# Optimization experiments

Hardware: AMD Instinct MI355X
Metric: run time of the kernel (lower is better)

## Reference

```python
import jax, jax.numpy as jnp
import numpy as np

N_NODES = 50000
D = 128
BN_EPS = 1e-5
GIN_EPS = 0.0  # GINConv default eps


def setup_inputs() -> dict:
    key = jax.random.key(0)
    ks = jax.random.split(key, 8)
    feature = jax.random.normal(ks[0], (N_NODES, D), dtype=jnp.float32)
    edge_index = jax.random.randint(ks[1], (2, 600000), 0, N_NODES, dtype=jnp.int32)
    s = 1.0 / np.sqrt(D)
    W1 = jax.random.uniform(ks[2], (D, D), jnp.float32, -s, s)
    b1 = jax.random.uniform(ks[3], (D,), jnp.float32, -s, s)
    W2 = jax.random.uniform(ks[4], (D, D), jnp.float32, -s, s)
    b2 = jax.random.uniform(ks[5], (D,), jnp.float32, -s, s)
    gamma = jnp.ones((D,), jnp.float32)
    beta = jnp.zeros((D,), jnp.float32)
    return {"feature": feature, "edge_index": edge_index,
            "W1": W1, "b1": b1, "W2": W2, "b2": b2,
            "gamma": gamma, "beta": beta}


def reference(feature, edge_index, W1, b1, W2, b2, gamma, beta):
    src, dst = edge_index[0], edge_index[1]
    # GIN aggregation: sum of neighbor (source) features at each target node
    agg = jax.ops.segment_sum(feature[src], dst, num_segments=N_NODES)
    h = (1.0 + GIN_EPS) * feature + agg
    # 2-layer MLP
    h = jax.nn.relu(h @ W1 + b1) @ W2 + b2
    # outer ReLU
    y = jax.nn.relu(h)
    # BatchNorm1d (training mode: batch statistics, biased variance)
    mean = jnp.mean(y, axis=0)
    var = jnp.mean(jnp.square(y - mean), axis=0)
    out = (y - mean) * jax.lax.rsqrt(var + BN_EPS) * gamma + beta
    return out
```

## Files before the change

kernel.cpp:

```cpp
#include <hip/hip_runtime.h>

#define N_NODES 50000
#define D 128
#define N_EDGES 600000
#define BN_EPS 1e-5f
#define NREP 64
#define BUCKET 64

#define MLP_BLOCKS 512
#define MLP_WAVES  (MLP_BLOCKS * 4)
#define N_GROUPS   3125

#define FEATC_BLOCKS 3125
#define WPREP_BLOCKS 128
#define ZERO_BLOCKS  260

typedef __attribute__((ext_vector_type(8))) short short8;
typedef __attribute__((ext_vector_type(4))) float floatx4;

__device__ __forceinline__ unsigned f2bf(float f) {
    unsigned x = __float_as_uint(f);
    return (x + 0x7fffu + ((x >> 16) & 1u)) >> 16;
}
__device__ __forceinline__ float bflo(unsigned v) { return __uint_as_float(v << 16); }
__device__ __forceinline__ float bfhi(unsigned v) { return __uint_as_float(v & 0xffff0000u); }

__global__ void prep_kernel(const float* __restrict__ f, unsigned* __restrict__ fb,
                            const float* __restrict__ W1, const float* __restrict__ W2,
                            unsigned short* __restrict__ Wt1, unsigned short* __restrict__ Wt2,
                            int* __restrict__ cnt, float* __restrict__ stats) {
    int b = blockIdx.x;
    int tid = threadIdx.x;
    if (b < FEATC_BLOCKS) {
        int gid = b * 256 + tid;
        float4 a = ((const float4*)f)[gid * 2];
        float4 c = ((const float4*)f)[gid * 2 + 1];
        uint4 o;
        o.x = f2bf(a.x) | (f2bf(a.y) << 16);
        o.y = f2bf(a.z) | (f2bf(a.w) << 16);
        o.z = f2bf(c.x) | (f2bf(c.y) << 16);
        o.w = f2bf(c.z) | (f2bf(c.w) << 16);
        ((uint4*)fb)[gid] = o;
    } else if (b < FEATC_BLOCKS + WPREP_BLOCKS) {
        int gid = (b - FEATC_BLOCKS) * 256 + tid;
        int m = gid >> 14;
        int idx = gid & (D * D - 1);
        int k = idx >> 7;
        int n = idx & 127;
        const float* W = m ? W2 : W1;
        unsigned short* Wt = m ? Wt2 : Wt1;
        Wt[n * D + k] = (unsigned short)f2bf(W[k * D + n]);
    } else {
        int gid = (b - FEATC_BLOCKS - WPREP_BLOCKS) * 256 + tid;
        if (gid < N_NODES) cnt[gid] = 0;
        int sid = gid - N_NODES;
        if (sid >= 0 && sid < NREP * 256) stats[sid] = 0.f;
    }
}

__global__ void scatter_kernel(const int* __restrict__ ei,
                               int* __restrict__ cnt,
                               unsigned short* __restrict__ ssrc) {
    int e = blockIdx.x * blockDim.x + threadIdx.x;
    if (e >= N_EDGES) return;
    int src = ei[e];
    int dst = ei[N_EDGES + e];
    int pos = atomicAdd(&cnt[dst], 1);
    ssrc[dst * BUCKET + pos] = (unsigned short)src;
}

__global__ __launch_bounds__(256) void gather_kernel(const uint4* __restrict__ fb4,
                                                     const int* __restrict__ cnt,
                                                     const unsigned short* __restrict__ ssrc,
                                                     uint4* __restrict__ hb4) {
    int wave = (blockIdx.x * 256 + threadIdx.x) >> 6;
    int lane = threadIdx.x & 63;
    int quad = lane >> 4;
    int l16 = lane & 15;
    int node = wave * 4 + quad;
    int beg = node * BUCKET;
    int end = beg + cnt[node];

    uint4 own = fb4[node * 16 + l16];
    float a0 = bflo(own.x), a1 = bfhi(own.x);
    float a2 = bflo(own.y), a3 = bfhi(own.y);
    float a4 = bflo(own.z), a5 = bfhi(own.z);
    float a6 = bflo(own.w), a7 = bfhi(own.w);

    int j = beg;
    #define ACC8(v) do { \
        a0 += bflo((v).x); a1 += bfhi((v).x); \
        a2 += bflo((v).y); a3 += bfhi((v).y); \
        a4 += bflo((v).z); a5 += bfhi((v).z); \
        a6 += bflo((v).w); a7 += bfhi((v).w); } while (0)
    for (; j + 7 < end; j += 8) {
        uint4 sv = *(const uint4*)&ssrc[j];
        int i0 = sv.x & 0xffff, i1 = sv.x >> 16;
        int i2 = sv.y & 0xffff, i3 = sv.y >> 16;
        int i4 = sv.z & 0xffff, i5 = sv.z >> 16;
        int i6 = sv.w & 0xffff, i7 = sv.w >> 16;
        uint4 v0 = fb4[i0 * 16 + l16];
        uint4 v1 = fb4[i1 * 16 + l16];
        uint4 v2 = fb4[i2 * 16 + l16];
        uint4 v3 = fb4[i3 * 16 + l16];
        uint4 v4 = fb4[i4 * 16 + l16];
        uint4 v5 = fb4[i5 * 16 + l16];
        uint4 v6 = fb4[i6 * 16 + l16];
        uint4 v7 = fb4[i7 * 16 + l16];
        ACC8(v0); ACC8(v1); ACC8(v2); ACC8(v3);
        ACC8(v4); ACC8(v5); ACC8(v6); ACC8(v7);
    }
    if (j + 3 < end) {
        ushort4 sv = *(const ushort4*)&ssrc[j];
        uint4 v0 = fb4[(int)sv.x * 16 + l16];
        uint4 v1 = fb4[(int)sv.y * 16 + l16];
        uint4 v2 = fb4[(int)sv.z * 16 + l16];
        uint4 v3 = fb4[(int)sv.w * 16 + l16];
        ACC8(v0); ACC8(v1); ACC8(v2); ACC8(v3);
        j += 4;
    }
    for (; j < end; ++j) {
        uint4 v = fb4[(int)ssrc[j] * 16 + l16];
        ACC8(v);
    }
    #undef ACC8

    uint4 o;
    o.x = f2bf(a0) | (f2bf(a1) << 16);
    o.y = f2bf(a2) | (f2bf(a3) << 16);
    o.z = f2bf(a4) | (f2bf(a5) << 16);
    o.w = f2bf(a6) | (f2bf(a7) << 16);
    hb4[node * 16 + l16] = o;
}

__global__ __launch_bounds__(256) void mlp_kernel(
    const unsigned short* __restrict__ A,
    const unsigned short* __restrict__ Bt1, const unsigned short* __restrict__ Bt2,
    const float* __restrict__ bias1, const float* __restrict__ bias2,
    unsigned short* __restrict__ yb, float* __restrict__ stats)
{
    __shared__ unsigned short B1lds[128 * 128];
    __shared__ unsigned short B2lds[128 * 128];
    __shared__ unsigned short Xch[4 * 16 * 128];

    const int tid = threadIdx.x;

    #pragma unroll
    for (int i = 0; i < 8; ++i) {
        int c = tid + i * 256;
        int row = c >> 4;
        int g = c & 15;
        int dst = row * 128 + (g ^ (row & 15)) * 8;
        int src = row * 128 + g * 8;
        *(uint4*)&B1lds[dst] = *(const uint4*)&Bt1[src];
        *(uint4*)&B2lds[dst] = *(const uint4*)&Bt2[src];
    }
    __syncthreads();

    const int lane = tid & 63;
    const int wid = tid >> 6;
    const int l15 = lane & 15;
    const int quad = lane >> 4;
    unsigned short* X = &Xch[wid * 2048];

    float bs1[8], bs2[8];
    #pragma unroll
    for (int n = 0; n < 8; ++n) {
        bs1[n] = bias1[n * 16 + l15];
        bs2[n] = bias2[n * 16 + l15];
    }

    float s[8], q[8];
    #pragma unroll
    for (int n = 0; n < 8; ++n) { s[n] = 0.f; q[n] = 0.f; }

    const int gw = blockIdx.x * 4 + wid;
    const int g1 = gw + MLP_WAVES;
    const bool has1 = (g1 < N_GROUPS);

    short8 afA[4], afB[4];
    #pragma unroll
    for (int kc = 0; kc < 4; ++kc)
        afA[kc] = *(const short8*)&A[(gw * 16 + l15) * 128 + kc * 32 + quad * 8];
    if (has1) {
        #pragma unroll
        for (int kc = 0; kc < 4; ++kc)
            afB[kc] = *(const short8*)&A[(g1 * 16 + l15) * 128 + kc * 32 + quad * 8];
    }

    auto compute = [&](int rowBase, short8* af) {
        floatx4 acc[8];
        #pragma unroll
        for (int n = 0; n < 8; ++n) acc[n] = (floatx4){0.f, 0.f, 0.f, 0.f};
        #pragma unroll
        for (int kc = 0; kc < 4; ++kc) {
            int ga = (kc * 4 + quad) ^ l15;
            #pragma unroll
            for (int n = 0; n < 8; ++n) {
                short8 bf = *(const short8*)&B1lds[(n * 16 + l15) * 128 + ga * 8];
                acc[n] = __builtin_amdgcn_mfma_f32_16x16x32_bf16(af[kc], bf, acc[n], 0, 0, 0);
            }
        }

        #pragma unroll
        for (int n = 0; n < 8; ++n) {
            int col = n * 16 + l15;
            int gg = col >> 3;
            int o7 = col & 7;
            #pragma unroll
            for (int r = 0; r < 4; ++r) {
                int rl = quad * 4 + r;
                float v = fmaxf(acc[n][r] + bs1[n], 0.f);
                X[rl * 128 + ((gg ^ rl) * 8) + o7] = (unsigned short)f2bf(v);
            }
        }
        short8 hf[4];
        #pragma unroll
        for (int kc = 0; kc < 4; ++kc)
            hf[kc] = *(const short8*)&X[l15 * 128 + (((kc * 4 + quad) ^ l15) * 8)];

        #pragma unroll
        for (int n = 0; n < 8; ++n) acc[n] = (floatx4){0.f, 0.f, 0.f, 0.f};
        #pragma unroll
        for (int kc = 0; kc < 4; ++kc) {
            int ga = (kc * 4 + quad) ^ l15;
            #pragma unroll
            for (int n = 0; n < 8; ++n) {
                short8 bf = *(const short8*)&B2lds[(n * 16 + l15) * 128 + ga * 8];
                acc[n] = __builtin_amdgcn_mfma_f32_16x16x32_bf16(hf[kc], bf, acc[n], 0, 0, 0);
            }
        }

        #pragma unroll
        for (int n = 0; n < 8; ++n) {
            int col = n * 16 + l15;
            #pragma unroll
            for (int r = 0; r < 4; ++r) {
                int row = rowBase + quad * 4 + r;
                float v = fmaxf(acc[n][r] + bs2[n], 0.f);
                yb[row * 128 + col] = (unsigned short)f2bf(v);
                s[n] += v;
                q[n] += v * v;
            }
        }
    };

    compute(gw * 16, afA);
    if (has1) compute(g1 * 16, afB);

    #pragma unroll
    for (int n = 0; n < 8; ++n) {
        s[n] += __shfl_xor(s[n], 16);
        s[n] += __shfl_xor(s[n], 32);
        q[n] += __shfl_xor(q[n], 16);
        q[n] += __shfl_xor(q[n], 32);
    }
    __syncthreads();
    float* red = (float*)B1lds;
    if (lane < 16) {
        #pragma unroll
        for (int n = 0; n < 8; ++n) {
            red[wid * 128 + n * 16 + lane] = s[n];
            red[512 + wid * 128 + n * 16 + lane] = q[n];
        }
    }
    __syncthreads();
    float* myStats = stats + (blockIdx.x & (NREP - 1)) * 256;
    if (tid < 128) {
        float ss = 0.f, qq = 0.f;
        #pragma unroll
        for (int w = 0; w < 4; ++w) {
            ss += red[w * 128 + tid];
            qq += red[512 + w * 128 + tid];
        }
        atomicAdd(&myStats[tid], ss);
        atomicAdd(&myStats[128 + tid], qq);
    }
}

__global__ __launch_bounds__(256) void bn_kernel(const uint4* __restrict__ yb4,
                                                 float* __restrict__ out,
                                                 const float* __restrict__ stats,
                                                 const float* __restrict__ gamma,
                                                 const float* __restrict__ beta)
{
    __shared__ float red[256];
    __shared__ float sc[128], sh[128];
    int tid = threadIdx.x;

    float acc = 0.f;
    #pragma unroll 8
    for (int r = 0; r < NREP; ++r) acc += stats[r * 256 + tid];
    red[tid] = acc;
    __syncthreads();
    if (tid < 128) {
        const float inv_n = 1.0f / (float)N_NODES;
        float m = red[tid] * inv_n;
        float var = red[128 + tid] * inv_n - m * m;
        float scale = gamma[tid] * rsqrtf(var + BN_EPS);
        sc[tid] = scale;
        sh[tid] = beta[tid] - m * scale;
    }
    __syncthreads();

    const int n8 = N_NODES * D / 8;
    int base = (blockIdx.x * 256 + tid) * 4;
    #pragma unroll
    for (int i = 0; i < 4; ++i) {
        int idx = base + i;
        if (idx >= n8) break;
        int c0 = (idx << 3) & 127;
        uint4 v = yb4[idx];
        float4 o0, o1;
        o0.x = bflo(v.x) * sc[c0 + 0] + sh[c0 + 0];
        o0.y = bfhi(v.x) * sc[c0 + 1] + sh[c0 + 1];
        o0.z = bflo(v.y) * sc[c0 + 2] + sh[c0 + 2];
        o0.w = bfhi(v.y) * sc[c0 + 3] + sh[c0 + 3];
        o1.x = bflo(v.z) * sc[c0 + 4] + sh[c0 + 4];
        o1.y = bfhi(v.z) * sc[c0 + 5] + sh[c0 + 5];
        o1.z = bflo(v.w) * sc[c0 + 6] + sh[c0 + 6];
        o1.w = bfhi(v.w) * sc[c0 + 7] + sh[c0 + 7];
        ((float4*)out)[idx * 2] = o0;
        ((float4*)out)[idx * 2 + 1] = o1;
    }
}

extern "C" void kernel_launch(void* const* d_in, const int* in_sizes, int n_in,
                              void* d_out, int out_size, void* d_ws, size_t ws_size,
                              hipStream_t stream) {
    const float* feature = (const float*)d_in[0];
    const int*   ei      = (const int*)d_in[1];
    const float* W1      = (const float*)d_in[2];
    const float* b1      = (const float*)d_in[3];
    const float* W2      = (const float*)d_in[4];
    const float* b2      = (const float*)d_in[5];
    const float* gamma   = (const float*)d_in[6];
    const float* beta    = (const float*)d_in[7];
    float* out = (float*)d_out;

    unsigned*       featb = (unsigned*)d_ws;
    unsigned*       hb    = featb + N_NODES * 64;
    unsigned*       yb32  = hb + N_NODES * 64;
    unsigned short* Wt1   = (unsigned short*)(yb32 + N_NODES * 64);
    unsigned short* Wt2   = Wt1 + D * D;
    float*          stats = (float*)(Wt2 + D * D);
    int*            cnt   = (int*)(stats + NREP * 256);
    unsigned short* ssrc  = (unsigned short*)(cnt + N_NODES);
    unsigned short* yb    = (unsigned short*)yb32;

    prep_kernel<<<FEATC_BLOCKS + WPREP_BLOCKS + ZERO_BLOCKS, 256, 0, stream>>>(
        feature, featb, W1, W2, Wt1, Wt2, cnt, stats);
    scatter_kernel<<<(N_EDGES + 255) / 256, 256, 0, stream>>>(ei, cnt, ssrc);
    gather_kernel<<<N_NODES / 4 * 64 / 256, 256, 0, stream>>>(
        (const uint4*)featb, cnt, ssrc, (uint4*)hb);
    mlp_kernel<<<MLP_BLOCKS, 256, 0, stream>>>(
        (const unsigned short*)hb, Wt1, Wt2, b1, b2, yb, stats);
    bn_kernel<<<(N_NODES * D / 8 / 4 + 255) / 256, 256, 0, stream>>>(
        (const uint4*)yb, out, stats, gamma, beta);
}
```

Measured before the change: 176.8 us.

## Replace global-atomic edge scatter with two-pass binned scatter using shared atomics

Edge bucketing now runs in two passes instead of one global atomicAdd per edge. The first kernel bins edges by destination block of 256 nodes, using shared-memory histograms and one global atomic per bin per block, and writes packed dst/src words. The second kernel processes each bin in one block, counting per-node slots with shared atomics so the ssrc and cnt writes stay localized. The number of BN statistics replicas also drops, which shrinks zeroing and the final reduction but may raise atomic contention in the MLP stats step. In exchange it adds a kernel launch and an intermediate buffer with a fixed capacity per bin.

Measured after the change: 157.7 us. 1.12x faster.

```diff
diff --git a/kernel.cpp b/kernel.cpp
--- a/kernel.cpp
+++ b/kernel.cpp
@@ -4,16 +4,21 @@
 #define D 128
 #define N_EDGES 600000
 #define BN_EPS 1e-5f
-#define NREP 64
+#define NREP 8
 #define BUCKET 64
 
 #define MLP_BLOCKS 512
 #define MLP_WAVES  (MLP_BLOCKS * 4)
 #define N_GROUPS   3125
 
+#define NBINS   196
+#define BINCAP  4096
+#define SA_EPB  2048
+#define SA_BLOCKS 293
+
 #define FEATC_BLOCKS 3125
 #define WPREP_BLOCKS 128
-#define ZERO_BLOCKS  260
+#define ZERO_BLOCKS  9
 
 typedef __attribute__((ext_vector_type(8))) short short8;
 typedef __attribute__((ext_vector_type(4))) float floatx4;
@@ -28,7 +33,7 @@
 __global__ void prep_kernel(const float* __restrict__ f, unsigned* __restrict__ fb,
                             const float* __restrict__ W1, const float* __restrict__ W2,
                             unsigned short* __restrict__ Wt1, unsigned short* __restrict__ Wt2,
-                            int* __restrict__ cnt, float* __restrict__ stats) {
+                            float* __restrict__ stats) {
     int b = blockIdx.x;
     int tid = threadIdx.x;
     if (b < FEATC_BLOCKS) {
@@ -51,22 +56,76 @@
         unsigned short* Wt = m ? Wt2 : Wt1;
         Wt[n * D + k] = (unsigned short)f2bf(W[k * D + n]);
     } else {
-        int gid = (b - FEATC_BLOCKS - WPREP_BLOCKS) * 256 + tid;
-        if (gid < N_NODES) cnt[gid] = 0;
-        int sid = gid - N_NODES;
-        if (sid >= 0 && sid < NREP * 256) stats[sid] = 0.f;
-    }
-}
-
-__global__ void scatter_kernel(const int* __restrict__ ei,
-                               int* __restrict__ cnt,
-                               unsigned short* __restrict__ ssrc) {
-    int e = blockIdx.x * blockDim.x + threadIdx.x;
-    if (e >= N_EDGES) return;
-    int src = ei[e];
-    int dst = ei[N_EDGES + e];
-    int pos = atomicAdd(&cnt[dst], 1);
-    ssrc[dst * BUCKET + pos] = (unsigned short)src;
+        int sid = (b - FEATC_BLOCKS - WPREP_BLOCKS) * 256 + tid;
+        if (sid < NREP * 256 + 256) stats[sid] = 0.f;
+    }
+}
+
+__global__ __launch_bounds__(256) void bin_scatter_a(const int* __restrict__ ei,
+                                                     int* __restrict__ binCnt,
+                                                     unsigned* __restrict__ binBuf) {
+    __shared__ int hist[NBINS];
+    __shared__ int base[NBINS];
+    const int tid = threadIdx.x;
+    for (int i = tid; i < NBINS; i += 256) hist[i] = 0;
+    __syncthreads();
+
+    const int e0 = blockIdx.x * SA_EPB;
+    const int nE = min(SA_EPB, N_EDGES - e0);
+
+    unsigned pk[8];
+    int lp[8];
+    int bn_[8];
+    #pragma unroll
+    for (int k = 0; k < 8; ++k) {
+        int idx = tid + k * 256;
+        if (idx < nE) {
+            int e = e0 + idx;
+            unsigned src = (unsigned)ei[e];
+            unsigned dst = (unsigned)ei[N_EDGES + e];
+            int bb = (int)(dst >> 8);
+            pk[k] = (dst << 16) | src;
+            bn_[k] = bb;
+            lp[k] = atomicAdd(&hist[bb], 1);
+        } else {
+            bn_[k] = -1;
+        }
+    }
+    __syncthreads();
+    for (int bb = tid; bb < NBINS; bb += 256) {
+        int h = hist[bb];
+        base[bb] = h ? atomicAdd(&binCnt[bb], h) : 0;
+    }
+    __syncthreads();
+    #pragma unroll
+    for (int k = 0; k < 8; ++k) {
+        if (bn_[k] >= 0)
+            binBuf[bn_[k] * BINCAP + base[bn_[k]] + lp[k]] = pk[k];
+    }
+}
+
+__global__ __launch_bounds__(1024) void bin_scatter_b(const unsigned* __restrict__ binBuf,
+                                                      const int* __restrict__ binCnt,
+                                                      int* __restrict__ cnt,
+                                                      unsigned short* __restrict__ ssrc) {
+    __shared__ int lcnt[256];
+    const int tid = threadIdx.x;
+    const int b = blockIdx.x;
+    if (tid < 256) lcnt[tid] = 0;
+    __syncthreads();
+
+    const int E = binCnt[b];
+    const unsigned* buf = binBuf + b * BINCAP;
+    for (int i = tid; i < E; i += 1024) {
+        unsigned p = buf[i];
+        int dst = (int)(p >> 16);
+        int src = (int)(p & 0xffffu);
+        int pos = atomicAdd(&lcnt[dst & 255], 1);
+        ssrc[dst * BUCKET + pos] = (unsigned short)src;
+    }
+    __syncthreads();
+    const int n0 = b << 8;
+    if (tid < 256 && n0 + tid < N_NODES) cnt[n0 + tid] = lcnt[tid];
 }
 
 __global__ __launch_bounds__(256) void gather_kernel(const uint4* __restrict__ fb4,
@@ -289,7 +348,7 @@
     int tid = threadIdx.x;
 
     float acc = 0.f;
-    #pragma unroll 8
+    #pragma unroll
     for (int r = 0; r < NREP; ++r) acc += stats[r * 256 + tid];
     red[tid] = acc;
     __syncthreads();
@@ -338,19 +397,22 @@
     const float* beta    = (const float*)d_in[7];
     float* out = (float*)d_out;
 
-    unsigned*       featb = (unsigned*)d_ws;
-    unsigned*       hb    = featb + N_NODES * 64;
-    unsigned*       yb32  = hb + N_NODES * 64;
-    unsigned short* Wt1   = (unsigned short*)(yb32 + N_NODES * 64);
-    unsigned short* Wt2   = Wt1 + D * D;
-    float*          stats = (float*)(Wt2 + D * D);
-    int*            cnt   = (int*)(stats + NREP * 256);
-    unsigned short* ssrc  = (unsigned short*)(cnt + N_NODES);
-    unsigned short* yb    = (unsigned short*)yb32;
+    unsigned*       featb  = (unsigned*)d_ws;
+    unsigned*       hb     = featb + N_NODES * 64;
+    unsigned*       yb32   = hb + N_NODES * 64;
+    unsigned short* Wt1    = (unsigned short*)(yb32 + N_NODES * 64);
+    unsigned short* Wt2    = Wt1 + D * D;
+    float*          stats  = (float*)(Wt2 + D * D);
+    int*            binCnt = (int*)(stats + NREP * 256);
+    int*            cnt    = binCnt + 256;
+    unsigned short* ssrc   = (unsigned short*)(cnt + N_NODES);
+    unsigned*       binBuf = (unsigned*)(ssrc + N_NODES * BUCKET);
+    unsigned short* yb     = (unsigned short*)yb32;
 
     prep_kernel<<<FEATC_BLOCKS + WPREP_BLOCKS + ZERO_BLOCKS, 256, 0, stream>>>(
-        feature, featb, W1, W2, Wt1, Wt2, cnt, stats);
-    scatter_kernel<<<(N_EDGES + 255) / 256, 256, 0, stream>>>(ei, cnt, ssrc);
+        feature, featb, W1, W2, Wt1, Wt2, stats);
+    bin_scatter_a<<<SA_BLOCKS, 256, 0, stream>>>(ei, binCnt, binBuf);
+    bin_scatter_b<<<NBINS, 1024, 0, stream>>>(binBuf, binCnt, cnt, ssrc);
     gather_kernel<<<N_NODES / 4 * 64 / 256, 256, 0, stream>>>(
         (const uint4*)featb, cnt, ssrc, (uint4*)hb);
     mlp_kernel<<<MLP_BLOCKS, 256, 0, stream>>>(
```
